# Kernel optimization log

Measured on AMD Instinct MI355X. Metric: run time of the kernel, lower is better.

## Reference

```python
import jax, jax.numpy as jnp
import numpy as np

N = 100000   # nodes
E = 3200000  # edges (avg degree 32)
K = 3        # num_stacks
L = 4        # num_layers (ARMA iterations)
H = 16       # hidden channels
C = 1        # num_classes
BN_EPS = 1e-5


def setup_inputs() -> dict:
    key = jax.random.key(0)
    ks = jax.random.split(key, 16)
    s = 0.1  # weight scale
    return {
        "x": jax.random.normal(ks[0], (N, 1), dtype=jnp.float32),
        "edge_index": jax.random.randint(ks[1], (2, E), 0, N, dtype=jnp.int64),
        "edge_attr": jax.random.uniform(ks[2], (E,), dtype=jnp.float32),
        "batch": jnp.zeros((N,), dtype=jnp.int64),
        # ARMAConv 1: 1 -> 16, shared weights
        "w1_init": s * jax.random.normal(ks[3], (K, 1, H), dtype=jnp.float32),
        "w1": s * jax.random.normal(ks[4], (K, H, H), dtype=jnp.float32),
        "w1_root": s * jax.random.normal(ks[5], (K, 1, H), dtype=jnp.float32),
        "b1": s * jax.random.normal(ks[6], (K, 1, H), dtype=jnp.float32),
        "bn1_g": jnp.ones((H,), dtype=jnp.float32),
        "bn1_b": jnp.zeros((H,), dtype=jnp.float32),
        # ARMAConv 2: 16 -> 1, shared weights, act=None
        "w2_init": s * jax.random.normal(ks[7], (K, H, C), dtype=jnp.float32),
        "w2": s * jax.random.normal(ks[8], (K, C, C), dtype=jnp.float32),
        "w2_root": s * jax.random.normal(ks[9], (K, H, C), dtype=jnp.float32),
        "b2": s * jax.random.normal(ks[10], (K, 1, C), dtype=jnp.float32),
    }


def _arma_conv(x, row, col, norm, w_init, w, w_root, b, n_layers, use_relu):
    """PyG ARMAConv with shared_weights=True, eval-mode dropout (identity).
    x: [N,Fin]; returns mean over K stacks: [N,Fout]."""
    n = x.shape[0]
    root = jnp.einsum('nf,kfo->kno', x, w_root)      # [K,N,Fout]
    out = jnp.einsum('nf,kfo->kno', x, w_init)       # [K,N,Fout]
    for t in range(n_layers):
        if t > 0:
            out = jnp.einsum('kno,kop->knp', out, w)
        # message: gather at source, scale by norm; aggregate (scatter-add) at target
        m = (out[:, row, :] * norm[None, :, None]).transpose(1, 0, 2)  # [E,K,F]
        out = jax.ops.segment_sum(m, col, num_segments=n).transpose(1, 0, 2)
        out = out + root + b
        if use_relu:
            out = jax.nn.relu(out)
    return out.mean(axis=0)


def reference(x, edge_index, edge_attr, batch, w1_init, w1, w1_root, b1,
              bn1_g, bn1_b, w2_init, w2, w2_root, b2):
    row, col = edge_index[0], edge_index[1]
    n = x.shape[0]
    # gcn_norm without self-loops: D^{-1/2} A D^{-1/2}
    deg = jax.ops.segment_sum(edge_attr, col, num_segments=n)
    dinv = jnp.where(deg > 0, jax.lax.rsqrt(jnp.maximum(deg, 1e-12)), 0.0)
    norm = dinv[row] * edge_attr * dinv[col]

    h = _arma_conv(x, row, col, norm, w1_init, w1, w1_root, b1, L, True)
    # BatchNorm1d (batch statistics) + ReLU; dropout is identity in eval
    mu = h.mean(axis=0)
    var = h.var(axis=0)
    h = (h - mu) * jax.lax.rsqrt(var + BN_EPS) * bn1_g + bn1_b
    h = jax.nn.relu(h)

    h = _arma_conv(h, row, col, norm, w2_init, w2, w2_root, b2, L, False)
    return jax.nn.sigmoid(h)
```

## Files before the change

kernel.cpp:

```cpp
#include <hip/hip_runtime.h>
#include <math.h>

#define N_NODES 100000
#define N_EDGES 3200000
#define KH 48
#define FDIM 64
#define NH 16
#define BN_EPS 1e-5f
#define NBUCK 196
#define BSHIFT 9
#define BMASK 511
#define EPB 16384
#define NBLK1 196
#define FIX 16777216.0f

typedef unsigned long long u64;
typedef unsigned int u32;
typedef unsigned short u16;

__device__ __forceinline__ u16 f2bf(float f) {
  u32 b = __float_as_uint(f);
  b += 0x7FFFu + ((b >> 16) & 1u);
  return (u16)(b >> 16);
}
__device__ __forceinline__ float bf2f(u32 s) {
  return __uint_as_float(s << 16);
}

__global__ __launch_bounds__(256) void bucket_count_kernel(
    const int* __restrict__ col, u32* __restrict__ btot ) {
  __shared__ u32 bins[NBUCK];
  for (int t = threadIdx.x; t < NBUCK; t += 256) bins[t] = 0;
  __syncthreads();
  int eb = blockIdx.x * EPB;
  for (int it = 0; it < EPB / 256; ++it) {
    int e = eb + it * 256 + threadIdx.x;
    if (e < N_EDGES) atomicAdd(&bins[col[e] >> BSHIFT], 1u);
  }
  __syncthreads();
  for (int t = threadIdx.x; t < NBUCK; t += 256)
    if (bins[t]) atomicAdd(&btot[t * 8], bins[t]);
}

__global__ __launch_bounds__(256) void bucket_scan_kernel(
    const u32* __restrict__ btot, u32* __restrict__ bstart, u32* __restrict__ gcur,
    int* __restrict__ offs) {
  __shared__ u32 sh[256];
  int t = threadIdx.x;
  u32 v = (t < NBUCK) ? btot[t * 8] : 0;
  sh[t] = v;
  __syncthreads();
  for (int d = 1; d < 256; d <<= 1) {
    u32 u = (t >= d) ? sh[t - d] : 0;
    __syncthreads();
    sh[t] += u;
    __syncthreads();
  }
  if (t < NBUCK) { u32 s = sh[t] - v; bstart[t] = s; gcur[t * 8] = s; }
  if (t == NBUCK) bstart[NBUCK] = N_EDGES;
  if (t == 0) offs[N_NODES] = N_EDGES;
}

__global__ __launch_bounds__(256) void bucket_scatter_kernel(
    const int* __restrict__ row, const int* __restrict__ col,
    const float* __restrict__ ea, u32* __restrict__ gcur,
    int2* __restrict__ bucketed) {
  __shared__ u32 bins[NBUCK];
  __shared__ u32 base[NBUCK];
  __shared__ u16 rnk[EPB];
  for (int t = threadIdx.x; t < NBUCK; t += 256) bins[t] = 0;
  __syncthreads();
  int eb = blockIdx.x * EPB;
  for (int it = 0; it < EPB / 256; ++it) {
    int i = it * 256 + threadIdx.x;
    int e = eb + i;
    if (e < N_EDGES) rnk[i] = (u16)atomicAdd(&bins[col[e] >> BSHIFT], 1u);
  }
  __syncthreads();
  for (int t = threadIdx.x; t < NBUCK; t += 256) {
    u32 c = bins[t];
    if (c) base[t] = atomicAdd(&gcur[t * 8], c);
  }
  __syncthreads();
  for (int it = 0; it < EPB / 256; ++it) {
    int i = it * 256 + threadIdx.x;
    int e = eb + i;
    if (e < N_EDGES) {
      int c = col[e];
      int bkt = c >> BSHIFT, cl = c & BMASK;
      u32 pos = base[bkt] + (u32)rnk[i];
      bucketed[pos] = make_int2((cl << 17) | row[e], __float_as_int(ea[e]));
    }
  }
}

__global__ __launch_bounds__(1024) void node_offs_kernel(
    const int2* __restrict__ bucketed, const u32* __restrict__ bstart,
    const float* __restrict__ x,
    int* __restrict__ offs, float* __restrict__ dinv, u16* __restrict__ zx) {
  __shared__ u32 cnt[512];
  __shared__ u32 degf[512];
  int t = threadIdx.x;
  if (t < 512) { cnt[t] = 0; degf[t] = 0; }
  __syncthreads();
  int b = blockIdx.x;
  u32 s = bstart[b], e = bstart[b + 1];
  for (u32 i = s + t; i < e; i += 1024) {
    int2 v = bucketed[i];
    int cl = (v.x >> 17) & BMASK;
    atomicAdd(&cnt[cl], 1u);
    atomicAdd(&degf[cl], (u32)(__int_as_float(v.y) * FIX));
  }
  __syncthreads();
  u32 v0 = (t < 512) ? cnt[t] : 0;
  for (int d = 1; d < 512; d <<= 1) {
    u32 u = (t < 512 && t >= d) ? cnt[t - d] : 0;
    __syncthreads();
    if (t < 512) cnt[t] += u;
    __syncthreads();
  }
  int n = b * 512 + t;
  if (t < 512 && n < N_NODES) {
    offs[n] = (int)(s + cnt[t] - v0);
    float dg = (float)degf[t] * (1.0f / FIX);
    float dv = dg > 0.f ? rsqrtf(fmaxf(dg, 1e-12f)) : 0.f;
    dinv[n] = dv;
    zx[n] = f2bf(x[n] * dv);
  }
}

__global__ __launch_bounds__(1024) void csr_fill_kernel(
    const int2* __restrict__ bucketed, const u32* __restrict__ bstart,
    const int* __restrict__ offs, u32* __restrict__ csr) {
  __shared__ u32 cur[512];
  int t = threadIdx.x;
  int b = blockIdx.x;
  int n = b * 512 + t;
  if (t < 512) cur[t] = (n < N_NODES) ? (u32)offs[n] : 0;
  __syncthreads();
  u32 s = bstart[b], e = bstart[b + 1];
  for (u32 i = s + t; i < e; i += 1024) {
    int2 v = bucketed[i];
    int cl = (v.x >> 17) & BMASK;
    u32 r = (u32)(v.x & 0x1FFFF);
    u16 w = f2bf(__int_as_float(v.y));
    u32 pos = atomicAdd(&cur[cl], 1u);
    csr[pos] = (r << 15) | (u32)w;
  }
}

__global__ __launch_bounds__(256) void sprop_kernel(
    const u32* __restrict__ csr, const int* __restrict__ offs,
    const u16* __restrict__ zx, const float* __restrict__ dinv,
    float* __restrict__ sbuf) {
  int t = blockIdx.x * 256 + threadIdx.x;
  int n = t >> 4, sub = t & 15;
  float a = 0.f;
  int s = offs[n], e = offs[n + 1];
  for (int i = s + sub; i < e; i += 16) {
    u32 ee = csr[i];
    a += bf2f(ee & 0x7FFFu) * bf2f((u32)zx[ee >> 15]);
  }
#pragma unroll
  for (int o = 8; o; o >>= 1) a += __shfl_xor(a, o, 64);
  if (sub == 0) sbuf[n] = dinv[n] * a;
}

__global__ __launch_bounds__(256) void conv1_mid_kernel(
    const float* __restrict__ sbuf, const float* __restrict__ x,
    const float* __restrict__ dinv,
    const float* __restrict__ w1i, const float* __restrict__ w1r,
    const float* __restrict__ b1, const float* __restrict__ w1,
    u16* __restrict__ tout) {
  int t = blockIdx.x * 256 + threadIdx.x;
  int n = t >> 4, c = t & 15;
  int base = (threadIdx.x & 63) & 48;
  float sn = sbuf[n], xn = x[n], dn = dinv[n];
#pragma unroll
  for (int k = 0; k < 3; ++k) {
    float u = fmaxf(sn * w1i[k * 16 + c] + xn * w1r[k * 16 + c] + b1[k * 16 + c], 0.f);
    float tf = 0.f;
#pragma unroll
    for (int f = 0; f < 16; ++f) tf += __shfl(u, base + f, 64) * w1[k * 256 + f * 16 + c];
    tout[(size_t)n * FDIM + k * 16 + c] = f2bf(tf * dn);
  }
}

__global__ __launch_bounds__(256) void conv1_prop_kernel(
    const u16* __restrict__ tin, u16* __restrict__ tout, float* __restrict__ hbuf,
    const u32* __restrict__ csr, const int* __restrict__ offs,
    const float* __restrict__ dinv, const float* __restrict__ x,
    const float* __restrict__ w1r, const float* __restrict__ b1,
    const float* __restrict__ w1, int do_t) {
  int lane = threadIdx.x & 63;
  int wid = (blockIdx.x * blockDim.x + threadIdx.x) >> 6;
  int nw = (gridDim.x * blockDim.x) >> 6;
  int c = lane;
  bool act = c < KH;
  float rb = act ? w1r[c] : 0.f;
  float bb = act ? b1[c] : 0.f;
  float wreg[16];
  if (do_t) {
    int k = c >> 4, o = c & 15;
    if (act) {
#pragma unroll
      for (int f = 0; f < 16; ++f) wreg[f] = w1[k * 256 + f * 16 + o];
    } else {
#pragma unroll
      for (int f = 0; f < 16; ++f) wreg[f] = 0.f;
    }
  }
  for (int n = wid; n < N_NODES; n += nw) {
    int nu = __builtin_amdgcn_readfirstlane(n);
    int s = offs[nu], e = offs[nu + 1];
    float acc = 0.f;
    int i = s;
    for (; i + 4 <= e; i += 4) {
      u32 e0 = csr[i], e1 = csr[i + 1], e2 = csr[i + 2], e3 = csr[i + 3];
      float v0 = 0.f, v1 = 0.f, v2 = 0.f, v3 = 0.f;
      if (act) {
        v0 = bf2f((u32)tin[(e0 >> 15) * FDIM + c]);
        v1 = bf2f((u32)tin[(e1 >> 15) * FDIM + c]);
        v2 = bf2f((u32)tin[(e2 >> 15) * FDIM + c]);
        v3 = bf2f((u32)tin[(e3 >> 15) * FDIM + c]);
      }
      acc += bf2f(e0 & 0x7FFFu) * v0 + bf2f(e1 & 0x7FFFu) * v1 +
             bf2f(e2 & 0x7FFFu) * v2 + bf2f(e3 & 0x7FFFu) * v3;
    }
    for (; i < e; ++i) {
      u32 ee = csr[i];
      if (act) acc += bf2f(ee & 0x7FFFu) * bf2f((u32)tin[(ee >> 15) * FDIM + c]);
    }
    float dn = dinv[nu];
    float u = fmaxf(acc * dn + x[nu] * rb + bb, 0.f);
    if (do_t) {
      float tf = 0.f;
      int base = c & 48;
#pragma unroll
      for (int f = 0; f < 16; ++f) tf += __shfl(u, base + f, 64) * wreg[f];
      if (act) tout[(size_t)nu * FDIM + c] = f2bf(tf * dn);
    } else {
      float m1v = __shfl(u, lane + 16, 64);
      float m2v = __shfl(u, lane + 32, 64);
      if (lane < NH) hbuf[(size_t)nu * NH + lane] = (u + m1v + m2v) * (1.f / 3.f);
    }
  }
}

__global__ __launch_bounds__(256) void bn_stats_kernel(
    const float* __restrict__ h, double* __restrict__ stats) {
  __shared__ float ssum[NH], ssq[NH];
  int tid = threadIdx.x;
  if (tid < NH) { ssum[tid] = 0.f; ssq[tid] = 0.f; }
  __syncthreads();
  int n = blockIdx.x * blockDim.x + tid;
  bool valid = n < N_NODES;
  const float4* p = (const float4*)(h + (size_t)(valid ? n : 0) * NH);
  float hv[NH];
#pragma unroll
  for (int q = 0; q < 4; ++q) {
    float4 v = valid ? p[q] : make_float4(0.f, 0.f, 0.f, 0.f);
    hv[q * 4 + 0] = v.x; hv[q * 4 + 1] = v.y; hv[q * 4 + 2] = v.z; hv[q * 4 + 3] = v.w;
  }
#pragma unroll
  for (int f = 0; f < NH; ++f) {
    float s = hv[f], q = hv[f] * hv[f];
    for (int o = 32; o; o >>= 1) { s += __shfl_xor(s, o, 64); q += __shfl_xor(q, o, 64); }
    if ((tid & 63) == 0) { atomicAdd(&ssum[f], s); atomicAdd(&ssq[f], q); }
  }
  __syncthreads();
  if (tid < NH) {
    atomicAdd(&stats[tid], (double)ssum[tid]);
    atomicAdd(&stats[NH + tid], (double)ssq[tid]);
  }
}

__global__ __launch_bounds__(64) void bn_final_kernel(
    const double* __restrict__ stats, const float* __restrict__ g,
    const float* __restrict__ b, float* __restrict__ sc, float* __restrict__ sh) {
  int f = threadIdx.x;
  if (f < NH) {
    double mu = stats[f] / (double)N_NODES;
    double var = stats[NH + f] / (double)N_NODES - mu * mu;
    float scale = g[f] * (float)(1.0 / sqrt(var + (double)BN_EPS));
    sc[f] = scale;
    sh[f] = b[f] - (float)mu * scale;
  }
}

__global__ __launch_bounds__(256) void conv2_init_kernel(
    const float* __restrict__ h, const float* __restrict__ sc, const float* __restrict__ sh,
    const float* __restrict__ dinv,
    const float* __restrict__ w2i, const float* __restrict__ w2r, const float* __restrict__ b2,
    float* __restrict__ P, float* __restrict__ R) {
  int n = blockIdx.x * blockDim.x + threadIdx.x;
  if (n >= N_NODES) return;
  float u[NH];
#pragma unroll
  for (int f = 0; f < NH; ++f) u[f] = fmaxf(h[(size_t)n * NH + f] * sc[f] + sh[f], 0.f);
  float dn = dinv[n];
#pragma unroll
  for (int k = 0; k < 3; ++k) {
    float r = b2[k], o = 0.f;
#pragma unroll
    for (int f = 0; f < NH; ++f) {
      r += u[f] * w2r[k * NH + f];
      o += u[f] * w2i[k * NH + f];
    }
    R[n * 4 + k] = r;
    P[n * 4 + k] = o * dn;
  }
  R[n * 4 + 3] = 0.f;
  P[n * 4 + 3] = 0.f;
}

__global__ __launch_bounds__(256) void conv2_prop_kernel(
    const float* __restrict__ in4, float* __restrict__ out4, float* __restrict__ y,
    const u32* __restrict__ csr, const int* __restrict__ offs,
    const float* __restrict__ dinv,
    const float* __restrict__ R, const float* __restrict__ w2,
    int scale_w2, int final_out) {
  int t = blockIdx.x * 256 + threadIdx.x;
  int n = t >> 4, sub = t & 15;
  float m0 = 1.f, m1 = 1.f, m2 = 1.f;
  if (scale_w2) { m0 = w2[0]; m1 = w2[1]; m2 = w2[2]; }
  int s = offs[n], e = offs[n + 1];
  float a0 = 0.f, a1 = 0.f, a2 = 0.f;
  for (int i = s + sub; i < e; i += 16) {
    u32 ee = csr[i];
    float w = bf2f(ee & 0x7FFFu);
    const float4 v = *(const float4*)(in4 + (size_t)(ee >> 15) * 4);
    a0 += w * v.x;
    a1 += w * v.y;
    a2 += w * v.z;
  }
#pragma unroll
  for (int o = 8; o; o >>= 1) {
    a0 += __shfl_xor(a0, o, 64);
    a1 += __shfl_xor(a1, o, 64);
    a2 += __shfl_xor(a2, o, 64);
  }
  if (sub == 0) {
    float dn = dinv[n];
    a0 = a0 * dn * m0 + R[n * 4 + 0];
    a1 = a1 * dn * m1 + R[n * 4 + 1];
    a2 = a2 * dn * m2 + R[n * 4 + 2];
    if (final_out) {
      float sm = (a0 + a1 + a2) * (1.f / 3.f);
      y[n] = 1.f / (1.f + expf(-sm));
    } else {
      out4[n * 4 + 0] = a0 * dn;
      out4[n * 4 + 1] = a1 * dn;
      out4[n * 4 + 2] = a2 * dn;
      out4[n * 4 + 3] = 0.f;
    }
  }
}

extern "C" void kernel_launch(void* const* d_in, const int* in_sizes, int n_in,
                              void* d_out, int out_size, void* d_ws, size_t ws_size,
                              hipStream_t stream) {
  const float* x   = (const float*)d_in[0];
  const int*   ei  = (const int*)d_in[1];
  const float* ea  = (const float*)d_in[2];
  const float* w1i = (const float*)d_in[4];
  const float* w1  = (const float*)d_in[5];
  const float* w1r = (const float*)d_in[6];
  const float* b1  = (const float*)d_in[7];
  const float* bng = (const float*)d_in[8];
  const float* bnb = (const float*)d_in[9];
  const float* w2i = (const float*)d_in[10];
  const float* w2  = (const float*)d_in[11];
  const float* w2r = (const float*)d_in[12];
  const float* b2  = (const float*)d_in[13];
  float* y = (float*)d_out;

  const int* row = ei;
  const int* col = ei + N_EDGES;

  char* ws = (char*)d_ws;
  size_t off = 0;
  auto alloc = [&](size_t bytes) -> char* {
    char* p = ws + off;
    off += (bytes + 255) & ~(size_t)255;
    return p;
  };
  u32*    btot   = (u32*)alloc((size_t)NBUCK * 8 * 4);
  u32*    gcur   = (u32*)alloc((size_t)NBUCK * 8 * 4);
  u32*    bstart = (u32*)alloc((size_t)(NBUCK + 1) * 4);
  int*    offs   = (int*)alloc((size_t)(N_NODES + 1) * 4);
  float*  dinv   = (float*)alloc((size_t)N_NODES * 4);
  u16*    zx     = (u16*)alloc((size_t)N_NODES * 2);
  float*  sbuf   = (float*)alloc((size_t)N_NODES * 4);
  double* stats  = (double*)alloc(32 * 8);
  float*  bnsc   = (float*)alloc(16 * 4);
  float*  bnsh   = (float*)alloc(16 * 4);
  int2*   bucketed = (int2*)alloc((size_t)N_EDGES * 8);
  u32*    csr    = (u32*)alloc((size_t)N_EDGES * 4);
  u16*    tA     = (u16*)alloc((size_t)N_NODES * FDIM * 2);
  u16*    tB     = (u16*)alloc((size_t)N_NODES * FDIM * 2);
  float*  hbuf   = (float*)alloc((size_t)N_NODES * NH * 4);
  float*  P2     = (float*)alloc((size_t)N_NODES * 4 * 4);
  float*  Q2     = (float*)alloc((size_t)N_NODES * 4 * 4);
  float*  R2     = (float*)alloc((size_t)N_NODES * 4 * 4);
  (void)ws_size; (void)in_sizes; (void)n_in; (void)out_size;

  hipMemsetAsync(btot, 0, (size_t)NBUCK * 8 * 4, stream);
  hipMemsetAsync(stats, 0, 32 * 8, stream);

  bucket_count_kernel<<<NBLK1, 256, 0, stream>>>(col, btot);
  bucket_scan_kernel<<<1, 256, 0, stream>>>(btot, bstart, gcur, offs);
  bucket_scatter_kernel<<<NBLK1, 256, 0, stream>>>(row, col, ea, gcur, bucketed);
  node_offs_kernel<<<NBUCK, 1024, 0, stream>>>(bucketed, bstart, x, offs, dinv, zx);
  csr_fill_kernel<<<NBUCK, 1024, 0, stream>>>(bucketed, bstart, offs, csr);

  const int NPB = 6250;
  sprop_kernel<<<NPB, 256, 0, stream>>>(csr, offs, zx, dinv, sbuf);
  conv1_mid_kernel<<<NPB, 256, 0, stream>>>(sbuf, x, dinv, w1i, w1r, b1, w1, tA);
  conv1_prop_kernel<<<4096, 256, 0, stream>>>(tA, tB, nullptr, csr, offs, dinv, x, w1r, b1, w1, 1);
  conv1_prop_kernel<<<4096, 256, 0, stream>>>(tB, tA, nullptr, csr, offs, dinv, x, w1r, b1, w1, 1);
  conv1_prop_kernel<<<4096, 256, 0, stream>>>(tA, nullptr, hbuf, csr, offs, dinv, x, w1r, b1, w1, 0);

  bn_stats_kernel<<<(N_NODES + 255) / 256, 256, 0, stream>>>(hbuf, stats);
  bn_final_kernel<<<1, 64, 0, stream>>>(stats, bng, bnb, bnsc, bnsh);
  conv2_init_kernel<<<(N_NODES + 255) / 256, 256, 0, stream>>>(
      hbuf, bnsc, bnsh, dinv, w2i, w2r, b2, P2, R2);

  conv2_prop_kernel<<<NPB, 256, 0, stream>>>(P2, Q2, nullptr, csr, offs, dinv, R2, w2, 0, 0);
  conv2_prop_kernel<<<NPB, 256, 0, stream>>>(Q2, P2, nullptr, csr, offs, dinv, R2, w2, 1, 0);
  conv2_prop_kernel<<<NPB, 256, 0, stream>>>(P2, Q2, nullptr, csr, offs, dinv, R2, w2, 1, 0);
  conv2_prop_kernel<<<NPB, 256, 0, stream>>>(Q2, P2, y, csr, offs, dinv, R2, w2, 1, 1);
}
```

Measured before the change: 560.4 us.

## Fuse CSR fill into node offsets kernel, add nontemporal CSR loads and 8-way unroll

Merges the node-offsets and CSR-fill kernels into one kernel that keeps per-node cursors in shared memory. This drops one launch and a second pass that re-read offsets. All CSR edge loads in the propagation kernels become nontemporal loads, so the streamed edge list does not evict the gathered feature rows from cache. The conv1 propagation inner loop also gains an 8-way unrolled path to keep more gathers in flight, at the cost of more registers.

```diff
diff --git a/kernel.cpp b/kernel.cpp
--- a/kernel.cpp
+++ b/kernel.cpp
@@ -94,12 +94,14 @@
   }
 }
 
-__global__ __launch_bounds__(1024) void node_offs_kernel(
+__global__ __launch_bounds__(1024) void node_build_kernel(
     const int2* __restrict__ bucketed, const u32* __restrict__ bstart,
     const float* __restrict__ x,
-    int* __restrict__ offs, float* __restrict__ dinv, u16* __restrict__ zx) {
+    int* __restrict__ offs, float* __restrict__ dinv, u16* __restrict__ zx,
+    u32* __restrict__ csr) {
   __shared__ u32 cnt[512];
   __shared__ u32 degf[512];
+  __shared__ u32 cur[512];
   int t = threadIdx.x;
   if (t < 512) { cnt[t] = 0; degf[t] = 0; }
   __syncthreads();
@@ -121,24 +123,15 @@
   }
   int n = b * 512 + t;
   if (t < 512 && n < N_NODES) {
-    offs[n] = (int)(s + cnt[t] - v0);
+    u32 o = s + cnt[t] - v0;
+    offs[n] = (int)o;
+    cur[t] = o;
     float dg = (float)degf[t] * (1.0f / FIX);
     float dv = dg > 0.f ? rsqrtf(fmaxf(dg, 1e-12f)) : 0.f;
     dinv[n] = dv;
     zx[n] = f2bf(x[n] * dv);
   }
-}
-
-__global__ __launch_bounds__(1024) void csr_fill_kernel(
-    const int2* __restrict__ bucketed, const u32* __restrict__ bstart,
-    const int* __restrict__ offs, u32* __restrict__ csr) {
-  __shared__ u32 cur[512];
-  int t = threadIdx.x;
-  int b = blockIdx.x;
-  int n = b * 512 + t;
-  if (t < 512) cur[t] = (n < N_NODES) ? (u32)offs[n] : 0;
-  __syncthreads();
-  u32 s = bstart[b], e = bstart[b + 1];
+  __syncthreads();
   for (u32 i = s + t; i < e; i += 1024) {
     int2 v = bucketed[i];
     int cl = (v.x >> 17) & BMASK;
@@ -158,7 +151,7 @@
   float a = 0.f;
   int s = offs[n], e = offs[n + 1];
   for (int i = s + sub; i < e; i += 16) {
-    u32 ee = csr[i];
+    u32 ee = __builtin_nontemporal_load(&csr[i]);
     a += bf2f(ee & 0x7FFFu) * bf2f((u32)zx[ee >> 15]);
   }
 #pragma unroll
@@ -215,8 +208,37 @@
     int s = offs[nu], e = offs[nu + 1];
     float acc = 0.f;
     int i = s;
+    for (; i + 8 <= e; i += 8) {
+      u32 e0 = __builtin_nontemporal_load(&csr[i]);
+      u32 e1 = __builtin_nontemporal_load(&csr[i + 1]);
+      u32 e2 = __builtin_nontemporal_load(&csr[i + 2]);
+      u32 e3 = __builtin_nontemporal_load(&csr[i + 3]);
+      u32 e4 = __builtin_nontemporal_load(&csr[i + 4]);
+      u32 e5 = __builtin_nontemporal_load(&csr[i + 5]);
+      u32 e6 = __builtin_nontemporal_load(&csr[i + 6]);
+      u32 e7 = __builtin_nontemporal_load(&csr[i + 7]);
+      float v0 = 0.f, v1 = 0.f, v2 = 0.f, v3 = 0.f;
+      float v4 = 0.f, v5 = 0.f, v6 = 0.f, v7 = 0.f;
+      if (act) {
+        v0 = bf2f((u32)tin[(e0 >> 15) * FDIM + c]);
+        v1 = bf2f((u32)tin[(e1 >> 15) * FDIM + c]);
+        v2 = bf2f((u32)tin[(e2 >> 15) * FDIM + c]);
+        v3 = bf2f((u32)tin[(e3 >> 15) * FDIM + c]);
+        v4 = bf2f((u32)tin[(e4 >> 15) * FDIM + c]);
+        v5 = bf2f((u32)tin[(e5 >> 15) * FDIM + c]);
+        v6 = bf2f((u32)tin[(e6 >> 15) * FDIM + c]);
+        v7 = bf2f((u32)tin[(e7 >> 15) * FDIM + c]);
+      }
+      acc += bf2f(e0 & 0x7FFFu) * v0 + bf2f(e1 & 0x7FFFu) * v1 +
+             bf2f(e2 & 0x7FFFu) * v2 + bf2f(e3 & 0x7FFFu) * v3 +
+             bf2f(e4 & 0x7FFFu) * v4 + bf2f(e5 & 0x7FFFu) * v5 +
+             bf2f(e6 & 0x7FFFu) * v6 + bf2f(e7 & 0x7FFFu) * v7;
+    }
     for (; i + 4 <= e; i += 4) {
-      u32 e0 = csr[i], e1 = csr[i + 1], e2 = csr[i + 2], e3 = csr[i + 3];
+      u32 e0 = __builtin_nontemporal_load(&csr[i]);
+      u32 e1 = __builtin_nontemporal_load(&csr[i + 1]);
+      u32 e2 = __builtin_nontemporal_load(&csr[i + 2]);
+      u32 e3 = __builtin_nontemporal_load(&csr[i + 3]);
       float v0 = 0.f, v1 = 0.f, v2 = 0.f, v3 = 0.f;
       if (act) {
         v0 = bf2f((u32)tin[(e0 >> 15) * FDIM + c]);
@@ -228,7 +250,7 @@
              bf2f(e2 & 0x7FFFu) * v2 + bf2f(e3 & 0x7FFFu) * v3;
     }
     for (; i < e; ++i) {
-      u32 ee = csr[i];
+      u32 ee = __builtin_nontemporal_load(&csr[i]);
       if (act) acc += bf2f(ee & 0x7FFFu) * bf2f((u32)tin[(ee >> 15) * FDIM + c]);
     }
     float dn = dinv[nu];
@@ -327,7 +349,7 @@
   int s = offs[n], e = offs[n + 1];
   float a0 = 0.f, a1 = 0.f, a2 = 0.f;
   for (int i = s + sub; i < e; i += 16) {
-    u32 ee = csr[i];
+    u32 ee = __builtin_nontemporal_load(&csr[i]);
     float w = bf2f(ee & 0x7FFFu);
     const float4 v = *(const float4*)(in4 + (size_t)(ee >> 15) * 4);
     a0 += w * v.x;
@@ -411,8 +433,7 @@
   bucket_count_kernel<<<NBLK1, 256, 0, stream>>>(col, btot);
   bucket_scan_kernel<<<1, 256, 0, stream>>>(btot, bstart, gcur, offs);
   bucket_scatter_kernel<<<NBLK1, 256, 0, stream>>>(row, col, ea, gcur, bucketed);
-  node_offs_kernel<<<NBUCK, 1024, 0, stream>>>(bucketed, bstart, x, offs, dinv, zx);
-  csr_fill_kernel<<<NBUCK, 1024, 0, stream>>>(bucketed, bstart, offs, csr);
+  node_build_kernel<<<NBUCK, 1024, 0, stream>>>(bucketed, bstart, x, offs, dinv, zx, csr);
 
   const int NPB = 6250;
   sprop_kernel<<<NPB, 256, 0, stream>>>(csr, offs, zx, dinv, sbuf);
```

New measurement: 553.8 us. Within noise of the previous version (-1.2%).
